# Performance work log

Hardware: AMD Instinct MI355X
Metric: run time of the kernel (lower is better)

Reference implementation:

```python
import jax, jax.numpy as jnp
import numpy as np
from jax import lax

K = 3  # AdaConv kernel_size inside conv_block


def conv2d(x, w, b, pad):
    # x: (B,C,H,W), w: (O,I,kh,kw) -> NCHW conv with symmetric padding
    y = lax.conv_general_dilated(x, w, (1, 1), [(pad, pad), (pad, pad)],
                                 dimension_numbers=('NCHW', 'OIHW', 'NCHW'))
    return y + b[None, :, None, None]


def unfold3(x):
    # nn.Unfold(kernel=3, pad=1): patches ordered channel-major then (kh,kw) row-major
    B, C, H, W = x.shape
    xp = jnp.pad(x, ((0, 0), (0, 0), (1, 1), (1, 1)))
    return jnp.stack([xp[:, :, i:i + H, j:j + W]
                      for i in range(K) for j in range(K)], axis=2)  # (B,C,9,H,W)


def adaconv(x, mask, aw_w, aw_b, mt_w, mt_b, c_w, c_b):
    # groups=1, groups_channels=out_ch in this configuration
    weight = conv2d(mask, aw_w, aw_b, pad=2)          # (B, 9, H, W)
    x = conv2d(x, c_w, c_b, pad=1)                    # (B, out_ch, H, W)
    p = unfold3(x)                                    # (B, out_ch, 9, H, W)
    out = jnp.einsum('bkhw,bckhw->bchw', weight, p)   # per-pixel adaptive conv
    mask2 = conv2d(mask, mt_w, mt_b, pad=2)
    return out, mask2


def lrelu(x):
    return jax.nn.leaky_relu(x, 0.01)


def setup_inputs() -> dict:
    key = jax.random.key(0)
    ks = jax.random.split(key, 20)
    B, Cin, Cout, Mi, Mo, H, W = 2, 64, 64, 64, 64, 256, 256
    s = 0.05
    d = {
        'x': jax.random.normal(ks[0], (B, Cin, H, W), jnp.float32),
        'mask': jax.random.normal(ks[1], (B, Mi, H, W), jnp.float32),
        # AdaConv 1 (in_ch->out_ch, mask_in->mask_out)
        'aw1_w': jax.random.normal(ks[2], (K * K, Mi, 2 * K - 1, 2 * K - 1), jnp.float32) * s,
        'aw1_b': jax.random.normal(ks[3], (K * K,), jnp.float32) * s,
        'mt1_w': jax.random.normal(ks[4], (Mo, Mi, 2 * K - 1, 2 * K - 1), jnp.float32) * s,
        'mt1_b': jax.random.normal(ks[5], (Mo,), jnp.float32) * s,
        'c1_w': jax.random.normal(ks[6], (Cout, Cin, K, K), jnp.float32) * s,
        'c1_b': jax.random.normal(ks[7], (Cout,), jnp.float32) * s,
        # AdaConv 2 (out_ch->out_ch, mask_out->mask_out)
        'aw2_w': jax.random.normal(ks[8], (K * K, Mo, 2 * K - 1, 2 * K - 1), jnp.float32) * s,
        'aw2_b': jax.random.normal(ks[9], (K * K,), jnp.float32) * s,
        'mt2_w': jax.random.normal(ks[10], (Mo, Mo, 2 * K - 1, 2 * K - 1), jnp.float32) * s,
        'mt2_b': jax.random.normal(ks[11], (Mo,), jnp.float32) * s,
        'c2_w': jax.random.normal(ks[12], (Cout, Cout, K, K), jnp.float32) * s,
        'c2_b': jax.random.normal(ks[13], (Cout,), jnp.float32) * s,
        # 1x1 residual conv
        'cr_w': jax.random.normal(ks[14], (Cout, Cin, 1, 1), jnp.float32) * s,
        'cr_b': jax.random.normal(ks[15], (Cout,), jnp.float32) * s,
    }
    return d


def reference(x, mask, aw1_w, aw1_b, mt1_w, mt1_b, c1_w, c1_b,
              aw2_w, aw2_b, mt2_w, mt2_b, c2_w, c2_b, cr_w, cr_b):
    res = conv2d(x, cr_w, cr_b, pad=0)
    x, mask = adaconv(x, mask, aw1_w, aw1_b, mt1_w, mt1_b, c1_w, c1_b)
    x, mask = lrelu(x), lrelu(mask)
    x, mask = adaconv(x, mask, aw2_w, aw2_b, mt2_w, mt2_b, c2_w, c2_b)
    x, mask = lrelu(x), lrelu(mask)
    return (x + res, mask)
```

## Files before the change

### kernel.cpp

```cpp
#include <hip/hip_runtime.h>

#define HWSZ 65536
#define CCH  64

typedef __bf16 bf16x8 __attribute__((ext_vector_type(8)));
typedef __bf16 bf16x4 __attribute__((ext_vector_type(4)));
typedef float  f32x4  __attribute__((ext_vector_type(4)));

__device__ inline void gload_lds16(const void* g, void* l) {
    __builtin_amdgcn_global_load_lds(
        (const __attribute__((address_space(1))) void*)g,
        (__attribute__((address_space(3))) void*)l, 16, 0, 0);
}


__device__ void cvt_body(int cb, const float* __restrict__ src,
                         __bf16* __restrict__ dst)
{
    int p  = cb * 256 + threadIdx.x;
    int b  = p >> 16, hw = p & 65535;
    const float* sp = src + (((size_t)b * 64) << 16) + hw;
    __bf16* dp = dst + (size_t)p * 64;
    #pragma unroll
    for (int c8 = 0; c8 < 8; ++c8) {
        bf16x8 v8;
        #pragma unroll
        for (int j = 0; j < 8; ++j)
            v8[j] = (__bf16)sp[(size_t)(c8 * 8 + j) << 16];
        *(bf16x8*)(dp + c8 * 8) = v8;
    }
}

__device__ void prep3_body(int cb, const float* __restrict__ src,
                           __bf16* __restrict__ dst)
{
    int t = cb * 256 + threadIdx.x;
    if (t >= 2 * 9 * 2048) return;
    int j  = t & 7;
    int u  = (t >> 3) & 255;
    int q  = t >> 11;
    int k  = q % 9, ci = q / 9;
    int r  = u >> 3;
    int v  = (u & 7) ^ (r & 7);
    int o  = 2 * r + (v >> 2);
    int g  = v & 3;
    int i  = ci * 32 + g * 8 + j;
    dst[t] = (__bf16)src[((size_t)o * 64 + i) * 9 + k];
}

__device__ void prepF_body(int cb, const float* __restrict__ mt,
                           const float* __restrict__ aw, __bf16* __restrict__ dst)
{
    int t = cb * 256 + threadIdx.x;
    if (t >= 2 * 25 * 3072) return;
    int j  = t & 7;
    int u  = (t >> 3) % 384;
    int q  = t / 3072;
    int k  = q % 25, ci = q / 25;
    int r  = u >> 3;
    int v  = (u & 7) ^ (r & 7);
    int o  = 2 * r + (v >> 2);
    int g  = v & 3;
    int i  = ci * 32 + g * 8 + j;
    float val = 0.f;
    if (o < 64)      val = mt[((size_t)o * 64 + i) * 25 + k];
    else if (o < 73) val = aw[((size_t)(o - 64) * 64 + i) * 25 + k];
    dst[t] = (__bf16)val;
}

__device__ void conv1x1p_body(float* lwT, float* lb, int cb,
    const float* __restrict__ x, const float* __restrict__ w,
    const float* __restrict__ bias, __bf16* __restrict__ res)
{
    int t = threadIdx.x;
    for (int s = t; s < 4096; s += 256) lwT[s] = w[(s & 63) * 64 + (s >> 6)];
    if (t < 64) lb[t] = bias[t];
    __syncthreads();

    int p  = cb * 256 + t;
    int b  = p >> 16, hw = p & 65535;
    const float* xp = x + (((size_t)b * 64) << 16) + hw;

    float acc[64];
    #pragma unroll
    for (int o = 0; o < 64; ++o) acc[o] = lb[o];

    #pragma unroll 4
    for (int i = 0; i < 64; ++i) {
        float xi = xp[(size_t)i << 16];
        const float4* w4 = (const float4*)&lwT[i * 64];
        #pragma unroll
        for (int o4 = 0; o4 < 16; ++o4) {
            float4 wv = w4[o4];
            acc[o4*4+0] += wv.x * xi;
            acc[o4*4+1] += wv.y * xi;
            acc[o4*4+2] += wv.z * xi;
            acc[o4*4+3] += wv.w * xi;
        }
    }
    __bf16* op = res + (((size_t)b * 64) << 16) + hw;
    #pragma unroll
    for (int o = 0; o < 64; ++o) op[(size_t)o << 16] = (__bf16)acc[o];
}

__global__ __launch_bounds__(256) void k_prep(
    const float* x, const float* mask,
    const float* c1w, const float* c2w,
    const float* mt1w, const float* aw1w,
    const float* mt2w, const float* aw2w,
    const float* crw, const float* crb,
    __bf16* xh, __bf16* mh, __bf16* resh,
    __bf16* wbc1, __bf16* wbc2, __bf16* wbF1, __bf16* wbF2)
{
    __shared__ __align__(16) float s1x1[4160];
    int bid = blockIdx.x;
    if      (bid < 512)  conv1x1p_body(s1x1, s1x1 + 4096, bid, x, crw, crb, resh);
    else if (bid < 1024) cvt_body(bid - 512, x, xh);
    else if (bid < 1536) cvt_body(bid - 1024, mask, mh);
    else if (bid < 1680) prep3_body(bid - 1536, c1w, wbc1);
    else if (bid < 1824) prep3_body(bid - 1680, c2w, wbc2);
    else if (bid < 2424) prepF_body(bid - 1824, mt1w, aw1w, wbF1);
    else                 prepF_body(bid - 2424, mt2w, aw2w, wbF2);
}

template<int EPI>
__global__ __launch_bounds__(256) void k_conv5(
    const __bf16* __restrict__ xh, const __bf16* __restrict__ wb,
    const float* __restrict__ bias, const float* __restrict__ bias2,
    float* __restrict__ outf, __bf16* __restrict__ outh,
    float* __restrict__ out2)
{
    constexpr int TW    = 20;
    constexpr int NPIX  = 400;
    constexpr int KK    = 25;
    constexpr int SROWS = 96;
    constexpr int SLICE = SROWS * 64;
    constexpr int NPIX2 = NPIX / 2;
    constexpr int MFT   = 5;

    __shared__ __align__(16) __bf16 lx[NPIX2 * 64];
    __shared__ __align__(16) __bf16 lw[2][SROWS * 32];
    __shared__ float lb[80];

    const int t    = threadIdx.x;
    const int w0   = blockIdx.x * 16, h0 = blockIdx.y * 16, b = blockIdx.z;
    const int wvv  = t >> 6;
    const int lane = t & 63;
    const int px   = lane & 15;
    const int g    = lane >> 4;

    auto STAGE = [&](int ci, int k, int buf) {
        const char* gs = (const char*)wb + (size_t)(ci * KK + k) * SLICE;
        if (wvv < 3) {
            #pragma unroll
            for (int r = 0; r < 2; ++r) {
                int ub = wvv * 128 + r * 64;
                gload_lds16(gs + (ub + lane) * 16, (char*)lw[buf] + ub * 16);
            }
        }
    };

    f32x4 acc[MFT][4];
    #pragma unroll
    for (int m = 0; m < MFT; ++m)
        #pragma unroll
        for (int nf = 0; nf < 4; ++nf)
            acc[m][nf] = (f32x4){0.f, 0.f, 0.f, 0.f};

    bf16x8 zv;
    #pragma unroll
    for (int j = 0; j < 8; ++j) zv[j] = (__bf16)0.f;

    for (int ci = 0; ci < 2; ++ci) {
        if (ci) __syncthreads();
        STAGE(ci, 0, 0);
        STAGE(ci, 1, 1);
        if (ci == 0) {
            if (t < 64) lb[t] = bias[t];
            if (t >= 64 && t < 80) lb[t] = (t - 64 < 9) ? bias2[t - 64] : 0.f;
        }

        #pragma unroll
        for (int xi = 0; xi < 7; ++xi) {
            int e = xi * 256 + t;
            if (e < NPIX * 4) {
                int pix = e >> 2, c4 = e & 3;
                int sy = pix / TW, sx = pix - sy * TW;
                int gy = h0 + sy - 2, gx = w0 + sx - 2;
                bool ok = (unsigned)gy < 256u && (unsigned)gx < 256u;
                bf16x8 v8 = zv;
                if (ok) v8 = *(const bf16x8*)(xh + ((((size_t)b << 16) + gy * 256 + gx) << 6)
                                              + ci * 32 + c4 * 8);
                int row = pix >> 1;
                int off = row * 128 + (((((pix & 1) << 2) + c4) ^ (row & 7)) << 4);
                *(bf16x8*)((char*)lx + off) = v8;
            }
        }
        __syncthreads();

        #pragma unroll
        for (int k = 0; k < KK; ++k) {
            const __bf16* lwb = (k & 1) ? lw[1] : lw[0];
            const int dy = k / 5, dx = k - dy * 5;

            bf16x8 bfr[4];
            #pragma unroll
            for (int nf = 0; nf < 4; ++nf) {
                int pix = (wvv * 4 + nf + dy) * TW + (px + dx);
                int row = pix >> 1;
                int off = row * 128 + (((((pix & 1) << 2) + g) ^ (row & 7)) << 4);
                bfr[nf] = *(const bf16x8*)((const char*)lx + off);
            }
            bf16x8 afr[MFT];
            #pragma unroll
            for (int m = 0; m < MFT; ++m) {
                int o = m * 16 + px;
                int row = o >> 1;
                int off = row * 128 + (((((o & 1) << 2) + g) ^ (row & 7)) << 4);
                afr[m] = *(const bf16x8*)((const char*)lwb + off);
            }
            __builtin_amdgcn_s_setprio(1);
            #pragma unroll
            for (int m = 0; m < MFT; ++m)
                #pragma unroll
                for (int nf = 0; nf < 4; ++nf)
                    acc[m][nf] = __builtin_amdgcn_mfma_f32_16x16x32_bf16(
                        afr[m], bfr[nf], acc[m][nf], 0, 0, 0);
            __builtin_amdgcn_s_setprio(0);

            if (k == KK - 1) break;

            asm volatile("s_waitcnt lgkmcnt(0)" ::: "memory");
            __builtin_amdgcn_sched_barrier(0);
            __builtin_amdgcn_s_barrier();
            bool issued = (k + 2 < KK);
            if (issued) STAGE(ci, k + 2, k & 1);
            if (issued && wvv < 3) asm volatile("s_waitcnt vmcnt(2)" ::: "memory");
            else                   asm volatile("s_waitcnt vmcnt(0)" ::: "memory");
            __builtin_amdgcn_sched_barrier(0);
            __builtin_amdgcn_s_barrier();
        }
    }

    #pragma unroll
    for (int m = 0; m < MFT; ++m) {
        #pragma unroll
        for (int nf = 0; nf < 4; ++nf) {
            int row = h0 + wvv * 4 + nf, col = w0 + px;
            if (m < 4) {
                float vj[4];
                #pragma unroll
                for (int j = 0; j < 4; ++j) {
                    float v = acc[m][nf][j] + lb[m * 16 + g * 4 + j];
                    vj[j] = v > 0.f ? v : 0.01f * v;
                }
                if constexpr (EPI == 0) {
                    bf16x4 pk;
                    #pragma unroll
                    for (int j = 0; j < 4; ++j) pk[j] = (__bf16)vj[j];
                    *(bf16x4*)(outh + ((((size_t)b << 16) + row * 256 + col) << 6)
                                    + m * 16 + g * 4) = pk;
                } else {
                    #pragma unroll
                    for (int j = 0; j < 4; ++j)
                        outf[((size_t)(b * 64 + m * 16 + g * 4 + j) << 16)
                             + row * 256 + col] = vj[j];
                }
            } else {
                #pragma unroll
                for (int j = 0; j < 4; ++j) {
                    int o2 = g * 4 + j;
                    if (o2 < 9)
                        out2[((size_t)(b * 9 + o2) << 16) + row * 256 + col]
                            = acc[m][nf][j] + lb[64 + o2];
                }
            }
        }
    }
}

__global__ __launch_bounds__(256) void k_conv3(
    const __bf16* __restrict__ xh, const __bf16* __restrict__ wb,
    const float* __restrict__ bias, __bf16* __restrict__ outh)
{
    constexpr int TW    = 18;
    constexpr int NPIX  = 324;
    constexpr int NPIX2 = 162;

    __shared__ __align__(16) __bf16 lx[NPIX2 * 64];
    __shared__ __align__(16) __bf16 lw[9 * 2048];
    __shared__ float lb[64];

    const int t    = threadIdx.x;
    const int w0   = blockIdx.x * 16, h0 = blockIdx.y * 16, b = blockIdx.z;
    const int wvv  = t >> 6;
    const int lane = t & 63;
    const int px   = lane & 15;
    const int g    = lane >> 4;

    f32x4 acc[4][4];
    #pragma unroll
    for (int m = 0; m < 4; ++m)
        #pragma unroll
        for (int nf = 0; nf < 4; ++nf)
            acc[m][nf] = (f32x4){0.f, 0.f, 0.f, 0.f};

    bf16x8 zv;
    #pragma unroll
    for (int j = 0; j < 8; ++j) zv[j] = (__bf16)0.f;

    for (int ci = 0; ci < 2; ++ci) {
        if (ci) __syncthreads();
        {
            const char* gs = (const char*)wb + (size_t)ci * 9 * 4096;
            #pragma unroll
            for (int r = 0; r < 9; ++r) {
                int ub = r * 256 + wvv * 64;
                gload_lds16(gs + (ub + lane) * 16, (char*)lw + ub * 16);
            }
        }
        if (ci == 0 && t < 64) lb[t] = bias[t];

        #pragma unroll
        for (int xi = 0; xi < 6; ++xi) {
            int e = xi * 256 + t;
            if (e < NPIX * 4) {
                int pix = e >> 2, c4 = e & 3;
                int sy = pix / TW, sx = pix - sy * TW;
                int gy = h0 + sy - 1, gx = w0 + sx - 1;
                bool ok = (unsigned)gy < 256u && (unsigned)gx < 256u;
                bf16x8 v8 = zv;
                if (ok) v8 = *(const bf16x8*)(xh + ((((size_t)b << 16) + gy * 256 + gx) << 6)
                                              + ci * 32 + c4 * 8);
                int row = pix >> 1;
                int off = row * 128 + (((((pix & 1) << 2) + c4) ^ (row & 7)) << 4);
                *(bf16x8*)((char*)lx + off) = v8;
            }
        }
        __syncthreads();

        #pragma unroll
        for (int k = 0; k < 9; ++k) {
            const __bf16* lwb = lw + k * 2048;
            const int dy = k / 3, dx = k - dy * 3;

            bf16x8 bfr[4];
            #pragma unroll
            for (int nf = 0; nf < 4; ++nf) {
                int pix = (wvv * 4 + nf + dy) * TW + (px + dx);
                int row = pix >> 1;
                int off = row * 128 + (((((pix & 1) << 2) + g) ^ (row & 7)) << 4);
                bfr[nf] = *(const bf16x8*)((const char*)lx + off);
            }
            bf16x8 afr[4];
            #pragma unroll
            for (int m = 0; m < 4; ++m) {
                int o = m * 16 + px;
                int row = o >> 1;
                int off = row * 128 + (((((o & 1) << 2) + g) ^ (row & 7)) << 4);
                afr[m] = *(const bf16x8*)((const char*)lwb + off);
            }
            __builtin_amdgcn_s_setprio(1);
            #pragma unroll
            for (int m = 0; m < 4; ++m)
                #pragma unroll
                for (int nf = 0; nf < 4; ++nf)
                    acc[m][nf] = __builtin_amdgcn_mfma_f32_16x16x32_bf16(
                        afr[m], bfr[nf], acc[m][nf], 0, 0, 0);
            __builtin_amdgcn_s_setprio(0);
        }
    }

    #pragma unroll
    for (int m = 0; m < 4; ++m) {
        #pragma unroll
        for (int nf = 0; nf < 4; ++nf) {
            int row = h0 + wvv * 4 + nf, col = w0 + px;
            bf16x4 pk;
            #pragma unroll
            for (int j = 0; j < 4; ++j) {
                float v = acc[m][nf][j] + lb[m * 16 + g * 4 + j];
                pk[j] = (__bf16)v;
            }
            *(bf16x4*)(outh + ((((size_t)b << 16) + row * 256 + col) << 6)
                            + m * 16 + g * 4) = pk;
        }
    }
}

__global__ __launch_bounds__(256, 4) void k_ada1(
    const float* __restrict__ wgt, const __bf16* __restrict__ xin,
    __bf16* __restrict__ outh)
{
    int t  = threadIdx.x;
    int pg = t >> 3, c8 = t & 7;
    int p  = blockIdx.x * 32 + pg;
    int b  = p >> 16, hw = p & 65535;
    int h  = hw >> 8, wc = hw & 255;

    const float* wp = wgt + ((size_t)(b * 9) << 16) + hw;
    const __bf16* cen = xin + (size_t)p * 64 + c8 * 8;

    float wk[9];
    const __bf16* nbp[9];
    #pragma unroll
    for (int dy = 0; dy < 3; ++dy)
        #pragma unroll
        for (int dx = 0; dx < 3; ++dx) {
            int k = dy * 3 + dx;
            bool ok = ((unsigned)(h + dy - 1) < 256u) &&
                      ((unsigned)(wc + dx - 1) < 256u);
            wk[k]  = ok ? wp[(size_t)k << 16] : 0.f;
            nbp[k] = ok ? cen + ((dy - 1) * 256 + (dx - 1)) * 64 : cen;
        }

    float acc[8] = {0.f,0.f,0.f,0.f,0.f,0.f,0.f,0.f};
    #pragma unroll
    for (int k = 0; k < 9; ++k) {
        bf16x8 v8 = *(const bf16x8*)nbp[k];
        float w = wk[k];
        #pragma unroll
        for (int j = 0; j < 8; ++j) acc[j] += w * (float)v8[j];
    }

    bf16x8 o8;
    #pragma unroll
    for (int j = 0; j < 8; ++j) {
        float v = acc[j];
        o8[j] = (__bf16)(v > 0.f ? v : 0.01f * v);
    }
    *(bf16x8*)(outh + (size_t)p * 64 + c8 * 8) = o8;
}

__global__ __launch_bounds__(256, 4) void k_ada2(
    const float* __restrict__ wgt, const __bf16* __restrict__ x2h,
    const __bf16* __restrict__ resh, float* __restrict__ outf)
{
    __shared__ float ls[32 * 65];

    int t  = threadIdx.x;
    int pg = t >> 3, c8 = t & 7;
    int p  = blockIdx.x * 32 + pg;
    int b  = p >> 16, hw = p & 65535;
    int h  = hw >> 8, wc = hw & 255;

    const float* wp = wgt + ((size_t)(b * 9) << 16) + hw;
    const __bf16* cen = x2h + (size_t)p * 64 + c8 * 8;

    float wk[9];
    const __bf16* nbp[9];
    #pragma unroll
    for (int dy = 0; dy < 3; ++dy)
        #pragma unroll
        for (int dx = 0; dx < 3; ++dx) {
            int k = dy * 3 + dx;
            bool ok = ((unsigned)(h + dy - 1) < 256u) &&
                      ((unsigned)(wc + dx - 1) < 256u);
            wk[k]  = ok ? wp[(size_t)k << 16] : 0.f;
            nbp[k] = ok ? cen + ((dy - 1) * 256 + (dx - 1)) * 64 : cen;
        }

    float acc[8] = {0.f,0.f,0.f,0.f,0.f,0.f,0.f,0.f};
    #pragma unroll
    for (int k = 0; k < 9; ++k) {
        bf16x8 v8 = *(const bf16x8*)nbp[k];
        float w = wk[k];
        #pragma unroll
        for (int j = 0; j < 8; ++j) acc[j] += w * (float)v8[j];
    }

    #pragma unroll
    for (int j = 0; j < 8; ++j) {
        float v = acc[j];
        ls[pg * 65 + c8 * 8 + j] = v > 0.f ? v : 0.01f * v;
    }
    __syncthreads();

    int pbase = blockIdx.x * 32;
    int bb    = pbase >> 16, hwb = pbase & 65535;
    int pix   = t & 31, cq = t >> 5;
    #pragma unroll
    for (int i = 0; i < 8; ++i) {
        int c = i * 8 + cq;
        size_t oi = ((size_t)(bb * 64 + c) << 16) + hwb + pix;
        outf[oi] = ls[pix * 65 + c] + (float)resh[oi];
    }
}

extern "C" void kernel_launch(void* const* d_in, const int* in_sizes, int n_in,
                              void* d_out, int out_size, void* d_ws, size_t ws_size,
                              hipStream_t stream)
{
    const float* x     = (const float*)d_in[0];
    const float* mask  = (const float*)d_in[1];
    const float* aw1_w = (const float*)d_in[2];
    const float* aw1_b = (const float*)d_in[3];
    const float* mt1_w = (const float*)d_in[4];
    const float* mt1_b = (const float*)d_in[5];
    const float* c1_w  = (const float*)d_in[6];
    const float* c1_b  = (const float*)d_in[7];
    const float* aw2_w = (const float*)d_in[8];
    const float* aw2_b = (const float*)d_in[9];
    const float* mt2_w = (const float*)d_in[10];
    const float* mt2_b = (const float*)d_in[11];
    const float* c2_w  = (const float*)d_in[12];
    const float* c2_b  = (const float*)d_in[13];
    const float* cr_w  = (const float*)d_in[14];
    const float* cr_b  = (const float*)d_in[15];

    float* out_x = (float*)d_out;
    float* out_m = (float*)d_out + 8388608;

    float*  wgt   = (float*)d_ws;
    __bf16* xh    = (__bf16*)((char*)d_ws + 4718592);
    __bf16* mh    = (__bf16*)((char*)d_ws + 21495808);
    __bf16* x2h   = mh;
    __bf16* wbase = (__bf16*)((char*)d_ws + 38273024);
    __bf16* wb_c1 = wbase;
    __bf16* wb_c2 = wbase + 36864;
    __bf16* wb_F1 = wbase + 73728;
    __bf16* wb_F2 = wbase + 227328;
    __bf16* resh  = (__bf16*)((char*)d_ws + 39034880);

    __bf16* maska_h = (__bf16*)out_x;
    __bf16* xa_h    = (__bf16*)out_x + 8388608;
    __bf16* x1_h    = (__bf16*)out_m;

    dim3 blk(256);
    dim3 gconv(16, 16, 2);
    dim3 gada(4096);

    k_prep<<<dim3(3024), blk, 0, stream>>>(x, mask, c1_w, c2_w,
        mt1_w, aw1_w, mt2_w, aw2_w, cr_w, cr_b,
        xh, mh, resh, wb_c1, wb_c2, wb_F1, wb_F2);

    k_conv5<0><<<gconv, blk, 0, stream>>>(mh, wb_F1, mt1_b, aw1_b,
                                          nullptr, maska_h, wgt);
    k_conv3<<<gconv, blk, 0, stream>>>(xh, wb_c1, c1_b, x1_h);
    k_ada1<<<gada, blk, 0, stream>>>(wgt, x1_h, xa_h);
    k_conv5<1><<<gconv, blk, 0, stream>>>(maska_h, wb_F2, mt2_b, aw2_b,
                                          out_m, nullptr, wgt);
    k_conv3<<<gconv, blk, 0, stream>>>(xa_h, wb_c2, c2_b, x2h);
    k_ada2<<<gada, blk, 0, stream>>>(wgt, x2h, resh, out_x);
}
```

Baseline: 186.3 us.

## Move residual 1x1 conv to MFMA kernel on channels-last bf16 input

Replaces the scalar FP32 1x1 residual convolution, which ran inside the prep kernel on NCHW fp32 input, with a separate MFMA-based k_conv1 kernel. The new kernel reads the already-converted channels-last bf16 x and writes the residual channels-last. k_ada2 now reads the residual per pixel as a contiguous bf16x8 vector and adds it before the LDS transpose, instead of reading it strided from NCHW. The cost is an extra kernel launch and a re-read of xh.

```diff
diff --git a/kernel.cpp b/kernel.cpp
--- a/kernel.cpp
+++ b/kernel.cpp
@@ -46,6 +46,22 @@
     int g  = v & 3;
     int i  = ci * 32 + g * 8 + j;
     dst[t] = (__bf16)src[((size_t)o * 64 + i) * 9 + k];
+}
+
+__device__ void prep1_body(int cb, const float* __restrict__ src,
+                           __bf16* __restrict__ dst)
+{
+    int t = cb * 256 + threadIdx.x;
+    if (t >= 2 * 2048) return;
+    int j  = t & 7;
+    int u  = (t >> 3) & 255;
+    int ci = t >> 11;
+    int r  = u >> 3;
+    int v  = (u & 7) ^ (r & 7);
+    int o  = 2 * r + (v >> 2);
+    int g  = v & 3;
+    int i  = ci * 32 + g * 8 + j;
+    dst[t] = (__bf16)src[(size_t)o * 64 + i];
 }
 
 __device__ void prepF_body(int cb, const float* __restrict__ mt,
@@ -68,59 +84,23 @@
     dst[t] = (__bf16)val;
 }
 
-__device__ void conv1x1p_body(float* lwT, float* lb, int cb,
-    const float* __restrict__ x, const float* __restrict__ w,
-    const float* __restrict__ bias, __bf16* __restrict__ res)
-{
-    int t = threadIdx.x;
-    for (int s = t; s < 4096; s += 256) lwT[s] = w[(s & 63) * 64 + (s >> 6)];
-    if (t < 64) lb[t] = bias[t];
-    __syncthreads();
-
-    int p  = cb * 256 + t;
-    int b  = p >> 16, hw = p & 65535;
-    const float* xp = x + (((size_t)b * 64) << 16) + hw;
-
-    float acc[64];
-    #pragma unroll
-    for (int o = 0; o < 64; ++o) acc[o] = lb[o];
-
-    #pragma unroll 4
-    for (int i = 0; i < 64; ++i) {
-        float xi = xp[(size_t)i << 16];
-        const float4* w4 = (const float4*)&lwT[i * 64];
-        #pragma unroll
-        for (int o4 = 0; o4 < 16; ++o4) {
-            float4 wv = w4[o4];
-            acc[o4*4+0] += wv.x * xi;
-            acc[o4*4+1] += wv.y * xi;
-            acc[o4*4+2] += wv.z * xi;
-            acc[o4*4+3] += wv.w * xi;
-        }
-    }
-    __bf16* op = res + (((size_t)b * 64) << 16) + hw;
-    #pragma unroll
-    for (int o = 0; o < 64; ++o) op[(size_t)o << 16] = (__bf16)acc[o];
-}
-
 __global__ __launch_bounds__(256) void k_prep(
     const float* x, const float* mask,
     const float* c1w, const float* c2w,
     const float* mt1w, const float* aw1w,
     const float* mt2w, const float* aw2w,
-    const float* crw, const float* crb,
-    __bf16* xh, __bf16* mh, __bf16* resh,
-    __bf16* wbc1, __bf16* wbc2, __bf16* wbF1, __bf16* wbF2)
-{
-    __shared__ __align__(16) float s1x1[4160];
+    const float* crw,
+    __bf16* xh, __bf16* mh,
+    __bf16* wbc1, __bf16* wbc2, __bf16* wbF1, __bf16* wbF2, __bf16* wbcr)
+{
     int bid = blockIdx.x;
-    if      (bid < 512)  conv1x1p_body(s1x1, s1x1 + 4096, bid, x, crw, crb, resh);
-    else if (bid < 1024) cvt_body(bid - 512, x, xh);
-    else if (bid < 1536) cvt_body(bid - 1024, mask, mh);
-    else if (bid < 1680) prep3_body(bid - 1536, c1w, wbc1);
-    else if (bid < 1824) prep3_body(bid - 1680, c2w, wbc2);
-    else if (bid < 2424) prepF_body(bid - 1824, mt1w, aw1w, wbF1);
-    else                 prepF_body(bid - 2424, mt2w, aw2w, wbF2);
+    if      (bid < 512)  cvt_body(bid, x, xh);
+    else if (bid < 1024) cvt_body(bid - 512, mask, mh);
+    else if (bid < 1168) prep3_body(bid - 1024, c1w, wbc1);
+    else if (bid < 1312) prep3_body(bid - 1168, c2w, wbc2);
+    else if (bid < 1912) prepF_body(bid - 1312, mt1w, aw1w, wbF1);
+    else if (bid < 2512) prepF_body(bid - 1912, mt2w, aw2w, wbF2);
+    else                 prep1_body(bid - 2512, crw, wbcr);
 }
 
 template<int EPI>
@@ -388,6 +368,91 @@
     }
 }
 
+__global__ __launch_bounds__(256) void k_conv1(
+    const __bf16* __restrict__ xh, const __bf16* __restrict__ wb,
+    const float* __restrict__ bias, __bf16* __restrict__ outh)
+{
+    constexpr int NPIX2 = 128;
+
+    __shared__ __align__(16) __bf16 lx[NPIX2 * 64];
+    __shared__ __align__(16) __bf16 lw[2048];
+    __shared__ float lb[64];
+
+    const int t    = threadIdx.x;
+    const int w0   = blockIdx.x * 16, h0 = blockIdx.y * 16, b = blockIdx.z;
+    const int wvv  = t >> 6;
+    const int lane = t & 63;
+    const int px   = lane & 15;
+    const int g    = lane >> 4;
+
+    f32x4 acc[4][4];
+    #pragma unroll
+    for (int m = 0; m < 4; ++m)
+        #pragma unroll
+        for (int nf = 0; nf < 4; ++nf)
+            acc[m][nf] = (f32x4){0.f, 0.f, 0.f, 0.f};
+
+    for (int ci = 0; ci < 2; ++ci) {
+        if (ci) __syncthreads();
+        {
+            const char* gs = (const char*)wb + (size_t)ci * 4096;
+            int ub = wvv * 64;
+            gload_lds16(gs + (ub + lane) * 16, (char*)lw + ub * 16);
+        }
+        if (ci == 0 && t < 64) lb[t] = bias[t];
+
+        #pragma unroll
+        for (int xi = 0; xi < 4; ++xi) {
+            int e = xi * 256 + t;
+            int pix = e >> 2, c4 = e & 3;
+            int gy = h0 + (pix >> 4), gx = w0 + (pix & 15);
+            bf16x8 v8 = *(const bf16x8*)(xh + ((((size_t)b << 16) + gy * 256 + gx) << 6)
+                                         + ci * 32 + c4 * 8);
+            int row = pix >> 1;
+            int off = row * 128 + (((((pix & 1) << 2) + c4) ^ (row & 7)) << 4);
+            *(bf16x8*)((char*)lx + off) = v8;
+        }
+        __syncthreads();
+
+        bf16x8 bfr[4];
+        #pragma unroll
+        for (int nf = 0; nf < 4; ++nf) {
+            int pix = (wvv * 4 + nf) * 16 + px;
+            int row = pix >> 1;
+            int off = row * 128 + (((((pix & 1) << 2) + g) ^ (row & 7)) << 4);
+            bfr[nf] = *(const bf16x8*)((const char*)lx + off);
+        }
+        bf16x8 afr[4];
+        #pragma unroll
+        for (int m = 0; m < 4; ++m) {
+            int o = m * 16 + px;
+            int row = o >> 1;
+            int off = row * 128 + (((((o & 1) << 2) + g) ^ (row & 7)) << 4);
+            afr[m] = *(const bf16x8*)((const char*)lw + off);
+        }
+        #pragma unroll
+        for (int m = 0; m < 4; ++m)
+            #pragma unroll
+            for (int nf = 0; nf < 4; ++nf)
+                acc[m][nf] = __builtin_amdgcn_mfma_f32_16x16x32_bf16(
+                    afr[m], bfr[nf], acc[m][nf], 0, 0, 0);
+    }
+
+    #pragma unroll
+    for (int m = 0; m < 4; ++m) {
+        #pragma unroll
+        for (int nf = 0; nf < 4; ++nf) {
+            int row = h0 + wvv * 4 + nf, col = w0 + px;
+            bf16x4 pk;
+            #pragma unroll
+            for (int j = 0; j < 4; ++j)
+                pk[j] = (__bf16)(acc[m][nf][j] + lb[m * 16 + g * 4 + j]);
+            *(bf16x4*)(outh + ((((size_t)b << 16) + row * 256 + col) << 6)
+                            + m * 16 + g * 4) = pk;
+        }
+    }
+}
+
 __global__ __launch_bounds__(256, 4) void k_ada1(
     const float* __restrict__ wgt, const __bf16* __restrict__ xin,
     __bf16* __restrict__ outh)
@@ -469,10 +534,12 @@
         for (int j = 0; j < 8; ++j) acc[j] += w * (float)v8[j];
     }
 
+    bf16x8 r8 = *(const bf16x8*)(resh + (size_t)p * 64 + c8 * 8);
     #pragma unroll
     for (int j = 0; j < 8; ++j) {
         float v = acc[j];
-        ls[pg * 65 + c8 * 8 + j] = v > 0.f ? v : 0.01f * v;
+        v = v > 0.f ? v : 0.01f * v;
+        ls[pg * 65 + c8 * 8 + j] = v + (float)r8[j];
     }
     __syncthreads();
 
@@ -483,7 +550,7 @@
     for (int i = 0; i < 8; ++i) {
         int c = i * 8 + cq;
         size_t oi = ((size_t)(bb * 64 + c) << 16) + hwb + pix;
-        outf[oi] = ls[pix * 65 + c] + (float)resh[oi];
+        outf[oi] = ls[pix * 65 + c];
     }
 }
 
@@ -520,7 +587,8 @@
     __bf16* wb_c2 = wbase + 36864;
     __bf16* wb_F1 = wbase + 73728;
     __bf16* wb_F2 = wbase + 227328;
-    __bf16* resh  = (__bf16*)((char*)d_ws + 39034880);
+    __bf16* wb_cr = wbase + 380928;
+    __bf16* resh  = (__bf16*)((char*)d_ws + 39043072);
 
     __bf16* maska_h = (__bf16*)out_x;
     __bf16* xa_h    = (__bf16*)out_x + 8388608;
@@ -530,9 +598,9 @@
     dim3 gconv(16, 16, 2);
     dim3 gada(4096);
 
-    k_prep<<<dim3(3024), blk, 0, stream>>>(x, mask, c1_w, c2_w,
-        mt1_w, aw1_w, mt2_w, aw2_w, cr_w, cr_b,
-        xh, mh, resh, wb_c1, wb_c2, wb_F1, wb_F2);
+    k_prep<<<dim3(2528), blk, 0, stream>>>(x, mask, c1_w, c2_w,
+        mt1_w, aw1_w, mt2_w, aw2_w, cr_w,
+        xh, mh, wb_c1, wb_c2, wb_F1, wb_F2, wb_cr);
 
     k_conv5<0><<<gconv, blk, 0, stream>>>(mh, wb_F1, mt1_b, aw1_b,
                                           nullptr, maska_h, wgt);
@@ -541,5 +609,6 @@
     k_conv5<1><<<gconv, blk, 0, stream>>>(maska_h, wb_F2, mt2_b, aw2_b,
                                           out_m, nullptr, wgt);
     k_conv3<<<gconv, blk, 0, stream>>>(xa_h, wb_c2, c2_b, x2h);
+    k_conv1<<<gconv, blk, 0, stream>>>(xh, wb_cr, cr_b, resh);
     k_ada2<<<gada, blk, 0, stream>>>(wgt, x2h, resh, out_x);
 }
```

After: 169.3 us. -9.1%, faster.
